# Kernel tuning notes

Measured on AMD Instinct MI355X. Metric: run time of the kernel, lower is better.

## Reference

```python
import jax, jax.numpy as jnp
import numpy as np
import math

N_HEADS = 16
THETA = 10000.0


def setup_inputs() -> dict:
    key = jax.random.key(0)
    ks = jax.random.split(key, 5)
    B, T, D = 4, 2048, 1024
    return {
        "x": jax.random.normal(ks[0], (B, T, D), dtype=jnp.float32),
        "w_qkv": jax.random.normal(ks[1], (3 * D, D), dtype=jnp.float32) * 0.02,
        "b_qkv": jax.random.normal(ks[2], (3 * D,), dtype=jnp.float32) * 0.02,
        "w_out": jax.random.normal(ks[3], (D, D), dtype=jnp.float32) * 0.02,
        "b_out": jax.random.normal(ks[4], (D,), dtype=jnp.float32) * 0.02,
    }


def reference(x, w_qkv, b_qkv, w_out, b_out):
    B, T, D = x.shape
    H = N_HEADS
    hd = D // H
    half = hd // 2

    # fused QKV projection (nn.Linear: y = x @ W^T + b)
    qkv = (x @ w_qkv.T + b_qkv).reshape(B, T, 3, H, hd)
    q, k, v = qkv[:, :, 0], qkv[:, :, 1], qkv[:, :, 2]

    # RoPE: interleaved (even, odd) pairs treated as complex, rotated by e^{i t w}
    inv_freq = 1.0 / (THETA ** (jnp.arange(0, hd, 2, dtype=jnp.float32) / hd))  # [half]
    angles = jnp.arange(T, dtype=jnp.float32)[:, None] * inv_freq[None, :]      # [T, half]
    cos = jnp.cos(angles)[None, :, None, :]  # [1,T,1,half]
    sin = jnp.sin(angles)[None, :, None, :]

    def rotate(t):
        tr = t.reshape(B, T, H, half, 2)
        te, to = tr[..., 0], tr[..., 1]
        rot = jnp.stack([te * cos - to * sin, te * sin + to * cos], axis=-1)
        return rot.reshape(B, T, H, hd).astype(t.dtype)

    q, k = rotate(q), rotate(k)

    # non-causal SDPA, scale = 1/sqrt(head_dim)
    scale = 1.0 / math.sqrt(hd)
    scores = jnp.einsum("bqhd,bkhd->bhqk", q, k) * scale
    attn = jax.nn.softmax(scores, axis=-1)
    out = jnp.einsum("bhqk,bkhd->bqhd", attn, v).reshape(B, T, D)

    return out @ w_out.T + b_out
```

## Files before the change

### kernel.cpp

```cpp
#include <hip/hip_runtime.h>

typedef __attribute__((ext_vector_type(4))) float f32x4;
typedef __attribute__((ext_vector_type(16))) float f32x16;
typedef __attribute__((ext_vector_type(8))) short bf16x8;
typedef __attribute__((ext_vector_type(4))) unsigned u32x4;

__device__ __forceinline__ unsigned short f2bf(float f) {
  unsigned u = __float_as_uint(f);
  u += 0x7fff + ((u >> 16) & 1);
  return (unsigned short)(u >> 16);
}
__device__ __forceinline__ float bf2f(unsigned short h) {
  return __uint_as_float(((unsigned)h) << 16);
}

__device__ __forceinline__ void gload_lds16(const void* g, void* lds) {
  __builtin_amdgcn_global_load_lds(
      (const __attribute__((address_space(1))) unsigned int*)g,
      (__attribute__((address_space(3))) unsigned int*)lds, 16, 0, 0);
}

__global__ void cast3_f32_bf16(const float* __restrict__ x,
                               const float* __restrict__ wq,
                               const float* __restrict__ wo,
                               unsigned short* __restrict__ xb,
                               unsigned short* __restrict__ wqb,
                               unsigned short* __restrict__ wob) {
  int i = blockIdx.x * blockDim.x + threadIdx.x;
  const float* src;
  unsigned short* dst;
  int off;
  if (i < 2097152) { src = x;  dst = xb;  off = i; }
  else if (i < 2883584) { src = wq; dst = wqb; off = i - 2097152; }
  else { src = wo; dst = wob; off = i - 2883584; }
  float4 v = ((const float4*)src)[off];
  ushort4 o;
  o.x = f2bf(v.x); o.y = f2bf(v.y); o.z = f2bf(v.z); o.w = f2bf(v.w);
  ((ushort4*)dst)[off] = o;
}

__global__ void rope_table(float2* __restrict__ cs) {
  int idx = blockIdx.x * blockDim.x + threadIdx.x;
  if (idx >= 2048 * 32) return;
  int t = idx >> 5, i = idx & 31;
  float inv = powf(10000.0f, -(float)(2 * i) / 64.0f);
  float a = (float)t * inv;
  cs[idx] = make_float2(cosf(a), sinf(a));
}

__global__ void rope_apply_k(unsigned short* __restrict__ qkv,
                             const float2* __restrict__ cs) {
  int idx = blockIdx.x * blockDim.x + threadIdx.x;
  int i = idx & 31;
  int h = (idx >> 5) & 15;
  int t = (idx >> 9) & 2047;
  int b = idx >> 20;
  float2 v = cs[(t << 5) | i];
  unsigned short* p =
      qkv + ((size_t)((b << 11) + t)) * 3072 + 1024 + h * 64 + 2 * i;
  unsigned pr = *(unsigned*)p;
  float e = bf2f((unsigned short)(pr & 0xffff));
  float o = bf2f((unsigned short)(pr >> 16));
  float ne = e * v.x - o * v.y;
  float no = e * v.y + o * v.x;
  *(unsigned*)p = (unsigned)f2bf(ne) | ((unsigned)f2bf(no) << 16);
}

template <int OUT_BF16>
__global__ __launch_bounds__(256, 2) void gemm_bt(
    const unsigned short* __restrict__ A, const unsigned short* __restrict__ B,
    const float* __restrict__ bias, void* __restrict__ Cout,
    int M, int N, int K) {
  __shared__ unsigned short lA[128 * 64];
  __shared__ unsigned short lB[128 * 64];
  const int tiles_n = N >> 7;
  const int swz = (blockIdx.x & 7) * (gridDim.x >> 3) + (blockIdx.x >> 3);
  const int bm = swz / tiles_n;
  const int bn = swz % tiles_n;
  const int tid = threadIdx.x;
  const int w = tid >> 6, l = tid & 63;
  const int l15 = l & 15, lq = l >> 4;
  const int wm = (w >> 1) * 64, wn = (w & 1) * 64;
  const int m0 = bm << 7, n0 = bn << 7;
  const int arow = l >> 3;
  const int acol = (l & 7) * 8;
  f32x4 acc[4][4] = {};

  for (int k0 = 0; k0 < K; k0 += 64) {
    __syncthreads();
#pragma unroll
    for (int it = 0; it < 4; ++it) {
      const int rb = it * 32 + w * 8;
      gload_lds16(A + (size_t)(m0 + rb + arow) * K + k0 + acol, &lA[rb * 64]);
      gload_lds16(B + (size_t)(n0 + rb + arow) * K + k0 + acol, &lB[rb * 64]);
    }
    __syncthreads();
#pragma unroll
    for (int ks = 0; ks < 2; ++ks) {
      bf16x8 af[4], bfr[4];
#pragma unroll
      for (int mi = 0; mi < 4; ++mi)
        af[mi] = *(const bf16x8*)&lA[(wm + mi * 16 + l15) * 64 + ks * 32 + lq * 8];
#pragma unroll
      for (int ni = 0; ni < 4; ++ni)
        bfr[ni] = *(const bf16x8*)&lB[(wn + ni * 16 + l15) * 64 + ks * 32 + lq * 8];
#pragma unroll
      for (int mi = 0; mi < 4; ++mi)
#pragma unroll
        for (int ni = 0; ni < 4; ++ni)
          acc[mi][ni] = __builtin_amdgcn_mfma_f32_16x16x32_bf16(
              af[mi], bfr[ni], acc[mi][ni], 0, 0, 0);
    }
  }

#pragma unroll
  for (int ni = 0; ni < 4; ++ni) {
    const int c = n0 + wn + ni * 16 + l15;
    const float bv = bias[c];
#pragma unroll
    for (int mi = 0; mi < 4; ++mi) {
#pragma unroll
      for (int j = 0; j < 4; ++j) {
        const int r = m0 + wm + mi * 16 + lq * 4 + j;
        const float v = acc[mi][ni][j] + bv;
        if (OUT_BF16)
          ((unsigned short*)Cout)[(size_t)r * N + c] = f2bf(v);
        else
          ((float*)Cout)[(size_t)r * N + c] = v;
      }
    }
  }
}


#define PACKPV(SCV, KS)                                                        \
  do {                                                                         \
    unsigned xa, xb, ya, yb;                                                   \
    asm("v_cvt_pk_bf16_f32 %0, %1, %2"                                         \
        : "=v"(xa) : "v"(SCV[((KS) & 1) * 8 + 0]), "v"(SCV[((KS) & 1) * 8 + 1])); \
    asm("v_cvt_pk_bf16_f32 %0, %1, %2"                                         \
        : "=v"(xb) : "v"(SCV[((KS) & 1) * 8 + 2]), "v"(SCV[((KS) & 1) * 8 + 3])); \
    asm("v_cvt_pk_bf16_f32 %0, %1, %2"                                         \
        : "=v"(ya) : "v"(SCV[((KS) & 1) * 8 + 4]), "v"(SCV[((KS) & 1) * 8 + 5])); \
    asm("v_cvt_pk_bf16_f32 %0, %1, %2"                                         \
        : "=v"(yb) : "v"(SCV[((KS) & 1) * 8 + 6]), "v"(SCV[((KS) & 1) * 8 + 7])); \
    asm("v_permlane32_swap_b32 %0, %1" : "+v"(xa), "+v"(ya));                  \
    asm("v_permlane32_swap_b32 %0, %1" : "+v"(xb), "+v"(yb));                  \
    u32x4 pw;                                                                  \
    pw[0] = xa; pw[1] = xb; pw[2] = ya; pw[3] = yb;                            \
    const bf16x8 pa = __builtin_bit_cast(bf16x8, pw);                          \
    {                                                                          \
      const bf16x8 vf = *(const bf16x8*)                                       \
          &lVc[l31 * 72 + ((16 * (KS) + 8 * hi) ^ (l31 & 0x30))];              \
      o0 = __builtin_amdgcn_mfma_f32_32x32x16_bf16(pa, vf, o0, 0, 0, 0);       \
    }                                                                          \
    {                                                                          \
      const int vrow = 32 + l31;                                               \
      const bf16x8 vf = *(const bf16x8*)                                       \
          &lVc[vrow * 72 + ((16 * (KS) + 8 * hi) ^ (vrow & 0x30))];            \
      o1 = __builtin_amdgcn_mfma_f32_32x32x16_bf16(pa, vf, o1, 0, 0, 0);       \
    }                                                                          \
  } while (0)

__global__ __launch_bounds__(512, 4) void attn_fwd(
    const unsigned short* __restrict__ qkv, unsigned short* __restrict__ aout,
    const float2* __restrict__ cs) {
  __shared__ unsigned short lK[2 * 64 * 64];
  __shared__ unsigned short lVt[2 * 64 * 72];

  const int g = blockIdx.x;
  const int xcd = g & 7;
  const int j2 = g >> 3;
  const int bh = ((j2 >> 3) << 3) + xcd;
  const int qt = j2 & 7;
  const int h = bh & 15, b = bh >> 4;

  const int tid = threadIdx.x;
  const int w = tid >> 6, l = tid & 63;
  const int l31 = l & 31, hi = l >> 5;
  const int l7 = l & 7;

  const size_t bt_base = (size_t)(b * 2048) * 3072;
  const int qbase = qt * 256 + w * 32;

  const unsigned short* Qp =
      qkv + bt_base + (size_t)(qbase + l31) * 3072 + h * 64 + hi * 8;
  const float2* csrow = cs + (size_t)(qbase + l31) * 32;
  bf16x8 qf[4];
#pragma unroll
  for (int s = 0; s < 4; ++s) {
    bf16x8 q = *(const bf16x8*)(Qp + 16 * s);
#pragma unroll
    for (int j = 0; j < 4; ++j) {
      const float2 cn = csrow[8 * s + 4 * hi + j];
      const float e = bf2f((unsigned short)q[2 * j]);
      const float o = bf2f((unsigned short)q[2 * j + 1]);
      q[2 * j]     = (short)f2bf((e * cn.x - o * cn.y) * 0.125f);
      q[2 * j + 1] = (short)f2bf((e * cn.y + o * cn.x) * 0.125f);
    }
    qf[s] = q;
  }

  const unsigned short* Kp = qkv + bt_base + 1024 + h * 64;
  const unsigned short* Vp = qkv + bt_base + 2048 + h * 64;

  const int krow = l >> 3;
  const int kcol = ((l & 7) ^ (l >> 3)) << 3;

  const int vr = tid >> 3;
  const int vc0 = (tid & 7) << 3;
  const int vx = vc0 & 0x30;

  f32x16 o0 = {}, o1 = {};
  float m_run = -1e30f, lsum = 0.f;
  bf16x8 v0;
  const float L2E = 1.4426950408889634f;

  {
    gload_lds16(Kp + (size_t)(w * 8 + krow) * 3072 + kcol, &lK[(w * 8) * 64]);
    const unsigned short* vb = Vp + (size_t)vr * 3072 + vc0;
    v0 = *(const bf16x8*)vb;
  }
  __syncthreads();
#pragma unroll
  for (int i2 = 0; i2 < 8; ++i2)
    lVt[(vc0 + i2) * 72 + (vr ^ vx)] = (unsigned short)v0[i2];
  __syncthreads();

  for (int t = 0; t < 32; ++t) {
    const int cur = t & 1;
    const unsigned short* lKc = lK + cur * 4096;
    const unsigned short* lVc = lVt + cur * 4608;
    const bool stage = (t < 31);

    if (stage) {
      const unsigned short* kb = Kp + (size_t)(t + 1) * 64 * 3072;
      gload_lds16(kb + (size_t)(w * 8 + krow) * 3072 + kcol,
                  lK + (cur ^ 1) * 4096 + (w * 8) * 64);
    }

    f32x16 s0 = {}, s1 = {};
    __builtin_amdgcn_s_setprio(1);
#pragma unroll
    for (int s = 0; s < 4; ++s) {
      bf16x8 kf = *(const bf16x8*)&lKc[l31 * 64 + (((2 * s + hi) ^ l7) << 3)];
      s0 = __builtin_amdgcn_mfma_f32_32x32x16_bf16(kf, qf[s], s0, 0, 0, 0);
    }
#pragma unroll
    for (int s = 0; s < 4; ++s) {
      bf16x8 kf = *(const bf16x8*)&lKc[(32 + l31) * 64 + (((2 * s + hi) ^ l7) << 3)];
      s1 = __builtin_amdgcn_mfma_f32_32x32x16_bf16(kf, qf[s], s1, 0, 0, 0);
    }
    __builtin_amdgcn_s_setprio(0);

    if (stage) {
      const unsigned short* vb =
          Vp + (size_t)(t + 1) * 64 * 3072 + (size_t)vr * 3072 + vc0;
      v0 = *(const bf16x8*)vb;
    }

    {
      float pmax = -1e30f;
#pragma unroll
      for (int r = 0; r < 16; r += 2) {
        float t0, t1;
        asm("v_max3_f32 %0, %1, %2, %3"
            : "=v"(t0) : "v"(s0[r]), "v"(s0[r + 1]), "v"(pmax));
        asm("v_max3_f32 %0, %1, %2, %3"
            : "=v"(t1) : "v"(s1[r]), "v"(s1[r + 1]), "v"(t0));
        pmax = t1;
      }
      pmax = fmaxf(pmax, __shfl_xor(pmax, 32));
      if (!__all(pmax <= m_run + 8.0f)) {
        const float mn = fmaxf(m_run, pmax);
        const float alpha = __expf(m_run - mn);
        m_run = mn;
        lsum *= alpha;
#pragma unroll
        for (int r = 0; r < 16; ++r) {
          const float ar = __shfl(alpha, (r & 3) + 8 * (r >> 2) + 4 * hi);
          o0[r] *= ar;
          o1[r] *= ar;
        }
      }
      const float m2 = m_run * L2E;
      float rsa = 0.f, rsb = 0.f;
#pragma unroll
      for (int r = 0; r < 16; r += 2) {
        float a0 = __builtin_fmaf(s0[r], L2E, -m2);
        float a1 = __builtin_fmaf(s0[r + 1], L2E, -m2);
        float p0, p1;
        asm("v_exp_f32 %0, %1" : "=v"(p0) : "v"(a0));
        asm("v_exp_f32 %0, %1" : "=v"(p1) : "v"(a1));
        s0[r] = p0; s0[r + 1] = p1; rsa += p0; rsb += p1;
        a0 = __builtin_fmaf(s1[r], L2E, -m2);
        a1 = __builtin_fmaf(s1[r + 1], L2E, -m2);
        asm("v_exp_f32 %0, %1" : "=v"(p0) : "v"(a0));
        asm("v_exp_f32 %0, %1" : "=v"(p1) : "v"(a1));
        s1[r] = p0; s1[r + 1] = p1; rsa += p0; rsb += p1;
      }
      float rs = rsa + rsb;
      rs += __shfl_xor(rs, 32);
      lsum += rs;
    }

    __builtin_amdgcn_s_setprio(1);
    PACKPV(s0, 0);
    PACKPV(s0, 1);
    PACKPV(s1, 2);
    PACKPV(s1, 3);
    __builtin_amdgcn_s_setprio(0);

    if (stage) {
      unsigned short* lVn = lVt + (cur ^ 1) * 4608;
#pragma unroll
      for (int i2 = 0; i2 < 8; ++i2)
        lVn[(vc0 + i2) * 72 + (vr ^ vx)] = (unsigned short)v0[i2];
    }
    __syncthreads();
  }

  const float linv = 1.0f / lsum;
#pragma unroll
  for (int r = 0; r < 16; ++r) {
    const int crow = (r & 3) + 8 * (r >> 2) + 4 * hi;
    const float lr = __shfl(linv, crow);
    unsigned short* orow =
        aout + (size_t)(b * 2048 + qbase + crow) * 1024 + h * 64 + l31;
    orow[0] = f2bf(o0[r] * lr);
    orow[32] = f2bf(o1[r] * lr);
  }
}

extern "C" void kernel_launch(void* const* d_in, const int* in_sizes, int n_in,
                              void* d_out, int out_size, void* d_ws, size_t ws_size,
                              hipStream_t stream) {
  const float* x     = (const float*)d_in[0];
  const float* w_qkv = (const float*)d_in[1];
  const float* b_qkv = (const float*)d_in[2];
  const float* w_out = (const float*)d_in[3];
  const float* b_out = (const float*)d_in[4];
  float* out = (float*)d_out;

  char* ws = (char*)d_ws;
  unsigned short* x_bf    = (unsigned short*)(ws);
  unsigned short* wqkv_bf = (unsigned short*)(ws + 16777216);
  unsigned short* wout_bf = (unsigned short*)(ws + 23068672);
  unsigned short* qkv     = (unsigned short*)(ws + 25165824);
  unsigned short* aout    = (unsigned short*)(ws + 75497472);
  float2* cs              = (float2*)(ws + 92274688);

  cast3_f32_bf16<<<3145728 / 256, 256, 0, stream>>>(x, w_qkv, w_out,
                                                    x_bf, wqkv_bf, wout_bf);
  rope_table<<<65536 / 256, 256, 0, stream>>>(cs);

  gemm_bt<1><<<64 * 24, 256, 0, stream>>>(x_bf, wqkv_bf, b_qkv, qkv,
                                          8192, 3072, 1024);
  rope_apply_k<<<4194304 / 256, 256, 0, stream>>>(qkv, cs);
  attn_fwd<<<512, 512, 0, stream>>>(qkv, aout, cs);
  gemm_bt<0><<<64 * 8, 256, 0, stream>>>(aout, wout_bf, b_out, out,
                                         8192, 1024, 1024);
}
```

Baseline: 209.9 us.

## Add 256x128-tile triple-buffered QKV GEMM with async LDS loads

Replaces the QKV projection GEMM with a new kernel that uses 256x128 output tiles, 512 threads, a three-stage LDS ring filled via direct global-to-LDS loads, XOR-swizzled layout, and a block-index swizzle for L2 locality. Each iteration waits with a partial vmcnt so loads for future K-steps overlap the MFMA work, and MFMA issue priority is raised. The aim is better data reuse per tile and load/compute overlap. In exchange it uses more LDS and registers per block, which may limit occupancy.

```diff
diff --git a/kernel.cpp b/kernel.cpp
--- a/kernel.cpp
+++ b/kernel.cpp
@@ -132,6 +132,104 @@
   }
 }
 
+__global__ __launch_bounds__(512, 2) void gemm_bt_p(
+    const unsigned short* __restrict__ A, const unsigned short* __restrict__ B,
+    const float* __restrict__ bias, unsigned short* __restrict__ Cout,
+    int M, int N, int K) {
+  __shared__ unsigned short lA[3 * 8192];
+  __shared__ unsigned short lB[3 * 4096];
+
+  const int tiles_n = N >> 7;
+  const int swz = (blockIdx.x & 7) * (gridDim.x >> 3) + (blockIdx.x >> 3);
+  const int bm = swz / tiles_n;
+  const int bn = swz % tiles_n;
+  const int m0 = bm << 8, n0 = bn << 7;
+  const int tid = threadIdx.x;
+  const int w = tid >> 6, l = tid & 63;
+  const int l15 = l & 15, lq = l >> 4;
+  const int wm = w >> 2, wn = w & 3;
+
+  const int sl8 = l >> 3, sc = l & 7;
+
+  f32x4 acc[8][2] = {};
+
+#define STAGE_HALF(J, RS)                                                     \
+  if ((J) < 32) {                                                             \
+    const int k0_ = (J) * 32;                                                 \
+    _Pragma("unroll")                                                         \
+    for (int i_ = 0; i_ < 2; ++i_) {                                          \
+      const int line = i_ * 64 + w * 8 + sl8;                                 \
+      const int lc = sc ^ (line & 7);                                         \
+      const int row = 2 * line + (lc >> 2);                                   \
+      gload_lds16(A + (size_t)(m0 + row) * K + k0_ + (lc & 3) * 8,            \
+                  &lA[(RS) * 8192 + line * 64 + sc * 8]);                     \
+    }                                                                         \
+    {                                                                         \
+      const int line = w * 8 + sl8;                                           \
+      const int lc = sc ^ (line & 7);                                         \
+      const int row = 2 * line + (lc >> 2);                                   \
+      gload_lds16(B + (size_t)(n0 + row) * K + k0_ + (lc & 3) * 8,            \
+                  &lB[(RS) * 4096 + line * 64 + sc * 8]);                     \
+    }                                                                         \
+  }
+
+  STAGE_HALF(0, 0);
+  STAGE_HALF(1, 1);
+
+  int rb = 0;
+  for (int j = 0; j < 32; ++j) {
+    if (j < 31)
+      asm volatile("s_waitcnt vmcnt(3)" ::: "memory");
+    else
+      asm volatile("s_waitcnt vmcnt(0)" ::: "memory");
+    __builtin_amdgcn_s_barrier();
+
+    bf16x8 af[8], bfr[2];
+#pragma unroll
+    for (int mi = 0; mi < 8; ++mi) {
+      const int row = wm * 128 + mi * 16 + l15;
+      const int line = row >> 1;
+      const int pc = (((row & 1) * 4 + lq) ^ (line & 7));
+      af[mi] = *(const bf16x8*)&lA[rb * 8192 + line * 64 + pc * 8];
+    }
+#pragma unroll
+    for (int ni = 0; ni < 2; ++ni) {
+      const int row = wn * 32 + ni * 16 + l15;
+      const int line = row >> 1;
+      const int pc = (((row & 1) * 4 + lq) ^ (line & 7));
+      bfr[ni] = *(const bf16x8*)&lB[rb * 4096 + line * 64 + pc * 8];
+    }
+
+    const int rs = rb == 0 ? 2 : rb - 1;
+    STAGE_HALF(j + 2, rs);
+
+    __builtin_amdgcn_s_setprio(1);
+#pragma unroll
+    for (int mi = 0; mi < 8; ++mi)
+#pragma unroll
+      for (int ni = 0; ni < 2; ++ni)
+        acc[mi][ni] = __builtin_amdgcn_mfma_f32_16x16x32_bf16(
+            af[mi], bfr[ni], acc[mi][ni], 0, 0, 0);
+    __builtin_amdgcn_s_setprio(0);
+
+    rb = rb == 2 ? 0 : rb + 1;
+  }
+#undef STAGE_HALF
+
+#pragma unroll
+  for (int ni = 0; ni < 2; ++ni) {
+    const int c = n0 + wn * 32 + ni * 16 + l15;
+    const float bv = bias[c];
+#pragma unroll
+    for (int mi = 0; mi < 8; ++mi) {
+#pragma unroll
+      for (int jj = 0; jj < 4; ++jj) {
+        const int r = m0 + wm * 128 + mi * 16 + lq * 4 + jj;
+        Cout[(size_t)r * N + c] = f2bf(acc[mi][ni][jj] + bv);
+      }
+    }
+  }
+}
 
 #define PACKPV(SCV, KS)                                                        \
   do {                                                                         \
@@ -354,8 +452,8 @@
                                                     x_bf, wqkv_bf, wout_bf);
   rope_table<<<65536 / 256, 256, 0, stream>>>(cs);
 
-  gemm_bt<1><<<64 * 24, 256, 0, stream>>>(x_bf, wqkv_bf, b_qkv, qkv,
-                                          8192, 3072, 1024);
+  gemm_bt_p<<<768, 512, 0, stream>>>(x_bf, wqkv_bf, b_qkv, qkv,
+                                     8192, 3072, 1024);
   rope_apply_k<<<4194304 / 256, 256, 0, stream>>>(qkv, cs);
   attn_fwd<<<512, 512, 0, stream>>>(qkv, aout, cs);
   gemm_bt<0><<<64 * 8, 256, 0, stream>>>(aout, wout_bf, b_out, out,
```

New measurement: 208.0 us. Within noise of the previous version (-0.9%).
